# Optimization experiments

Measured on AMD Instinct MI355X. Metric: run time of the kernel, lower is better.

## Reference

```python
import jax, jax.numpy as jnp
import numpy as np

N_NODES = 100000
N_EDGES = 1600000
N_GRAPHS = 1000
HID = 64
NEG_SLOPE = 0.2


def _glorot(key, shape):
    fan_in, fan_out = shape[0], shape[-1]
    lim = float(np.sqrt(6.0 / (fan_in + fan_out)))
    return jax.random.uniform(key, shape, jnp.float32, -lim, lim)


def setup_inputs() -> dict:
    key = jax.random.key(0)
    ks = jax.random.split(key, 20)
    x = jax.random.normal(ks[0], (N_NODES, 1), jnp.float32)
    edge_index = jax.random.randint(ks[1], (2, N_EDGES), 0, N_NODES, jnp.int64)
    batch = jnp.sort(jax.random.randint(ks[2], (N_NODES,), 0, N_GRAPHS, jnp.int64))
    inp = {"x": x, "edge_index": edge_index, "batch": batch}
    # GATv2Conv layer 1 (in=3 -> out=HID, 1 head)
    inp["Wl1"] = _glorot(ks[3], (3, HID)); inp["bl1"] = jnp.zeros((HID,), jnp.float32)
    inp["Wr1"] = _glorot(ks[4], (3, HID)); inp["br1"] = jnp.zeros((HID,), jnp.float32)
    inp["a1"] = _glorot(ks[5], (HID, 1))[:, 0]; inp["b1"] = jnp.zeros((HID,), jnp.float32)
    # GATv2Conv layer 2 (HID -> HID)
    inp["Wl2"] = _glorot(ks[6], (HID, HID)); inp["bl2"] = jnp.zeros((HID,), jnp.float32)
    inp["Wr2"] = _glorot(ks[7], (HID, HID)); inp["br2"] = jnp.zeros((HID,), jnp.float32)
    inp["a2"] = _glorot(ks[8], (HID, 1))[:, 0]; inp["b2"] = jnp.zeros((HID,), jnp.float32)
    # lin2 (HID -> 2)
    inp["W3"] = _glorot(ks[9], (HID, 2)); inp["b3"] = jnp.zeros((2,), jnp.float32)
    return inp


def gatv2_layer(x, src, dst, Wl, bl, Wr, br, a, b):
    """GATv2Conv, 1 head, add_self_loops=True, negative_slope=0.2."""
    n = x.shape[0]
    xl = x @ Wl + bl  # source-side transform [N, C]
    xr = x @ Wr + br  # target-side transform [N, C]
    loops = jnp.arange(n, dtype=src.dtype)
    s = jnp.concatenate([src, loops])
    d = jnp.concatenate([dst, loops])
    # per-edge attention logit: a^T LeakyReLU(xl[j] + xr[i])
    e = jax.nn.leaky_relu(xl[s] + xr[d], NEG_SLOPE) @ a  # [E+N]
    # segment softmax over incoming edges of each dst node
    m = jax.ops.segment_max(e, d, num_segments=n)
    ex = jnp.exp(e - m[d])
    denom = jax.ops.segment_sum(ex, d, num_segments=n)
    alpha = ex / denom[d]
    out = jax.ops.segment_sum(alpha[:, None] * xl[s], d, num_segments=n)
    return out + b


def reference(x, edge_index, batch, Wl1, bl1, Wr1, br1, a1, b1,
              Wl2, bl2, Wr2, br2, a2, b2, W3, b3):
    n = x.shape[0]
    src, dst = edge_index[0], edge_index[1]
    ones = jnp.ones((src.shape[0],), jnp.float32)
    deg_in = jax.ops.segment_sum(ones, dst, num_segments=n)   # bincount(dst)
    deg_out = jax.ops.segment_sum(ones, src, num_segments=n)  # bincount(src)
    h = jnp.concatenate([x, deg_in[:, None], deg_out[:, None]], axis=1)  # [N,3]
    h = gatv2_layer(h, src, dst, Wl1, bl1, Wr1, br1, a1, b1)
    h = jnp.tanh(h)
    h = gatv2_layer(h, src, dst, Wl2, bl2, Wr2, br2, a2, b2)
    # global_max_pool over graphs
    g = jax.ops.segment_max(h, batch, num_segments=N_GRAPHS)  # [G, HID]
    return g @ W3 + b3  # [G, 2]
```

## Files before the change

### kernel.cpp

```cpp
#include <hip/hip_runtime.h>
#include <hip/hip_bf16.h>
#include <hip/hip_fp16.h>

#define HID 64
#define NEG_SLOPE 0.2f
#define BLK_E 4096
#define EDGE_CAP 6144
#define NDB 16

typedef _Float16 f16x2 __attribute__((ext_vector_type(2)));


__global__ void k_hist2(const int* __restrict__ src, const int* __restrict__ dst,
                        int* __restrict__ histS, int* __restrict__ histD,
                        int E, int NB, int NBLK) {
    __shared__ int hs[512], hd[512];
    int t = threadIdx.x, blk = blockIdx.x;
    for (int b = t; b < NB; b += 1024) { hs[b] = 0; hd[b] = 0; }
    __syncthreads();
    int base = blk * BLK_E;
    #pragma unroll
    for (int k = 0; k < BLK_E / 1024; ++k) {
        int i = base + k * 1024 + t;
        if (i < E) {
            atomicAdd(&hs[src[i] >> 8], 1);
            atomicAdd(&hd[dst[i] >> 8], 1);
        }
    }
    __syncthreads();
    for (int b = t; b < NB; b += 1024) {
        histS[b * NBLK + blk] = hs[b];
        histD[b * NBLK + blk] = hd[b];
    }
}

__global__ void k_binscan(int* __restrict__ histS, int* __restrict__ histD,
                          int* __restrict__ totS, int* __restrict__ totD,
                          int NB, int NBLK) {
    __shared__ int s[512];
    int b = blockIdx.x;
    int* hist = histS; int* tot = totS;
    if (b >= NB) { b -= NB; hist = histD; tot = totD; }
    int t = threadIdx.x;
    int v = (t < NBLK) ? hist[b * NBLK + t] : 0;
    s[t] = v;
    __syncthreads();
    for (int o = 1; o < 512; o <<= 1) {
        int u = (t >= o) ? s[t - o] : 0;
        __syncthreads();
        s[t] += u;
        __syncthreads();
    }
    if (t < NBLK) hist[b * NBLK + t] = s[t] - v;
    if (t == 511) tot[b] = s[511];
}

__global__ void k_binoffset(const int* __restrict__ totS, const int* __restrict__ totD,
                            int* __restrict__ bsS, int* __restrict__ bsD,
                            int NB, int E, int* __restrict__ row_off, int N) {
    __shared__ int s[512];
    int t = threadIdx.x;
    int v = (t < NB) ? totS[t] : 0;
    s[t] = v; __syncthreads();
    for (int o = 1; o < 512; o <<= 1) {
        int u = (t >= o) ? s[t - o] : 0;
        __syncthreads(); s[t] += u; __syncthreads();
    }
    if (t < NB) bsS[t] = s[t] - v;
    if (t == 0) bsS[NB] = E;
    __syncthreads();
    v = (t < NB) ? totD[t] : 0;
    s[t] = v; __syncthreads();
    for (int o = 1; o < 512; o <<= 1) {
        int u = (t >= o) ? s[t - o] : 0;
        __syncthreads(); s[t] += u; __syncthreads();
    }
    if (t < NB) bsD[t] = s[t] - v;
    if (t == 0) { bsD[NB] = E; row_off[N] = E; }
}

__global__ void k_scatter_bins(const int* __restrict__ src, const int* __restrict__ dst,
                               const int* __restrict__ histS, const int* __restrict__ histD,
                               const int* __restrict__ bsS, const int* __restrict__ bsD,
                               unsigned* __restrict__ packS, unsigned* __restrict__ packD,
                               int E, int NB, int NBLK) {
    __shared__ int baseS[512], baseD[512];
    int t = threadIdx.x, blk = blockIdx.x;
    for (int b = t; b < NB; b += 1024) {
        baseS[b] = bsS[b] + histS[b * NBLK + blk];
        baseD[b] = bsD[b] + histD[b * NBLK + blk];
    }
    __syncthreads();
    int base = blk * BLK_E;
    #pragma unroll
    for (int k = 0; k < BLK_E / 1024; ++k) {
        int i = base + k * 1024 + t;
        if (i < E) {
            int sv = src[i], dv = dst[i];
            int pD = atomicAdd(&baseD[dv >> 8], 1);
            packD[pD] = ((unsigned)(dv & 255) << 24) | (unsigned)sv;
            int pS = atomicAdd(&baseS[sv >> 8], 1);
            packS[pS] = (unsigned)(sv & 255);
        }
    }
}

__global__ void k_csr_bin_fused(const unsigned* __restrict__ packD, const int* __restrict__ bsD,
                                const unsigned* __restrict__ packS, const int* __restrict__ bsS,
                                int* __restrict__ row_off, float* __restrict__ deg_in,
                                int* __restrict__ csr_src,
                                const float* __restrict__ x,
                                const float* __restrict__ Wl, const float* __restrict__ bl,
                                const float* __restrict__ Wr, const float* __restrict__ br,
                                __half* __restrict__ A, __half* __restrict__ B, int N) {
    __shared__ int cnt[256], off[256], cur[256], cntS[256];
    __shared__ unsigned eb[EDGE_CAP];
    int b = blockIdx.x, t = threadIdx.x;
    int lo = bsD[b], hi = bsD[b + 1], ne = hi - lo;
    bool fits = (ne <= EDGE_CAP);
    if (t < 256) { cnt[t] = 0; cntS[t] = 0; }
    __syncthreads();
    for (int i = t; i < ne; i += 1024) {
        unsigned v = packD[lo + i];
        if (fits) eb[i] = v;
        atomicAdd(&cnt[v >> 24], 1);
    }
    int loS = bsS[b], hiS = bsS[b + 1];
    for (int i = loS + t; i < hiS; i += 1024) atomicAdd(&cntS[packS[i] & 255], 1);
    __syncthreads();
    if (t < 256) off[t] = cnt[t];
    __syncthreads();
    for (int o = 1; o < 256; o <<= 1) {
        int u = 0;
        if (t < 256 && t >= o) u = off[t - o];
        __syncthreads();
        if (t < 256) off[t] += u;
        __syncthreads();
    }
    if (t < 256) {
        int ex = off[t] - cnt[t];
        cur[t] = lo + ex;
        int node = b * 256 + t;
        if (node < N) {
            row_off[node] = lo + ex;
            deg_in[node] = (float)cnt[t];
        }
    }
    __syncthreads();
    for (int i = t; i < ne; i += 1024) {
        unsigned v = fits ? eb[i] : packD[lo + i];
        int pos = atomicAdd(&cur[v >> 24], 1);
        csr_src[pos] = (int)(v & 0xFFFFFFu);
    }
    int nd = b * 256 + (t >> 2);
    if (nd < N) {
        float h0 = x[nd];
        float h1 = (float)cnt[t >> 2];
        float h2 = (float)cntS[t >> 2];
        int c0 = (t & 3) * 16;
        unsigned ua[4], ub[4];
        #pragma unroll
        for (int p = 0; p < 2; ++p) {
            #pragma unroll
            for (int q = 0; q < 4; ++q) {
                int c = c0 + p * 8 + q * 2;
                float a0 = h0 * Wl[c]     + h1 * Wl[64 + c]     + h2 * Wl[128 + c]     + bl[c];
                float a1 = h0 * Wl[c + 1] + h1 * Wl[64 + c + 1] + h2 * Wl[128 + c + 1] + bl[c + 1];
                float b0 = h0 * Wr[c]     + h1 * Wr[64 + c]     + h2 * Wr[128 + c]     + br[c];
                float b1 = h0 * Wr[c + 1] + h1 * Wr[64 + c + 1] + h2 * Wr[128 + c + 1] + br[c + 1];
                f16x2 pa; pa.x = (_Float16)a0; pa.y = (_Float16)a1;
                f16x2 pb; pb.x = (_Float16)b0; pb.y = (_Float16)b1;
                ua[q] = __builtin_bit_cast(unsigned, pa);
                ub[q] = __builtin_bit_cast(unsigned, pb);
            }
            uint4 sa = make_uint4(ua[0], ua[1], ua[2], ua[3]);
            uint4 sb = make_uint4(ub[0], ub[1], ub[2], ub[3]);
            ((uint4*)A)[(size_t)nd * 8 + (t & 3) * 2 + p] = sa;
            ((uint4*)B)[(size_t)nd * 8 + (t & 3) * 2 + p] = sb;
        }
    }
}


__global__ void k_deghist(const float* __restrict__ deg_in, int* __restrict__ dhist, int N) {
    __shared__ int h[64];
    int t = threadIdx.x, b = blockIdx.x;
    if (t < 64) h[t] = 0;
    __syncthreads();
    int chunk = (N + NDB - 1) / NDB;
    int lo = b * chunk, hi = lo + chunk; if (hi > N) hi = N;
    for (int i = lo + t; i < hi; i += 1024) {
        int dg = (int)deg_in[i]; if (dg > 63) dg = 63;
        atomicAdd(&h[dg], 1);
    }
    __syncthreads();
    if (t < 64) dhist[t * NDB + b] = h[t];
}

__global__ void k_degscan(int* __restrict__ dhist) {
    __shared__ int s[1024];
    int t = threadIdx.x;
    int v = dhist[t];
    s[t] = v; __syncthreads();
    for (int o = 1; o < 1024; o <<= 1) {
        int u = (t >= o) ? s[t - o] : 0;
        __syncthreads(); s[t] += u; __syncthreads();
    }
    dhist[t] = s[t] - v;
}

__global__ void k_degscatter(const float* __restrict__ deg_in, const int* __restrict__ dhist,
                             int* __restrict__ perm, int N) {
    __shared__ int cur[64];
    int t = threadIdx.x, b = blockIdx.x;
    if (t < 64) cur[t] = dhist[t * NDB + b];
    __syncthreads();
    int chunk = (N + NDB - 1) / NDB;
    int lo = b * chunk, hi = lo + chunk; if (hi > N) hi = N;
    for (int i = lo + t; i < hi; i += 1024) {
        int dg = (int)deg_in[i]; if (dg > 63) dg = 63;
        int p = atomicAdd(&cur[dg], 1);
        perm[p] = i;
    }
}


struct H4 { f16x2 h[4]; };

__device__ __forceinline__ f16x2 bch2(unsigned u) {
    return __builtin_bit_cast(f16x2, u);
}

__device__ __forceinline__ H4 ld4(const uint4* __restrict__ T, size_t idx) {
    uint4 r = T[idx];
    H4 o;
    o.h[0] = bch2(r.x); o.h[1] = bch2(r.y); o.h[2] = bch2(r.z); o.h[3] = bch2(r.w);
    return o;
}

__device__ __forceinline__ float logit8(const H4& a, const H4& x,
                                        const float* __restrict__ awf, f16x2 ns2) {
    float t = 0.0f;
    #pragma unroll
    for (int j = 0; j < 4; ++j) {
        f16x2 s = a.h[j] + x.h[j];
        f16x2 l = __builtin_elementwise_max(s, ns2 * s);
        t = fmaf((float)l.x, awf[2 * j], t);
        t = fmaf((float)l.y, awf[2 * j + 1], t);
    }
    return t;
}

__device__ __forceinline__ void accum8(float* __restrict__ acc, const H4& a, float w) {
    #pragma unroll
    for (int j = 0; j < 4; ++j) {
        acc[2 * j]     = fmaf((float)a.h[j].x, w, acc[2 * j]);
        acc[2 * j + 1] = fmaf((float)a.h[j].y, w, acc[2 * j + 1]);
    }
}

template <typename OUT, bool TANH>
__global__ void k_gat_fused(const int* __restrict__ csr_src, const int* __restrict__ row_off,
                            const int* __restrict__ perm,
                            const __half* __restrict__ Ah, const __half* __restrict__ Bh,
                            const float* __restrict__ aw, const float* __restrict__ bias,
                            OUT* __restrict__ out, int N) {
    int tid = blockIdx.x * blockDim.x + threadIdx.x;
    int r = tid >> 3;
    int gl = threadIdx.x & 7;
    if (r >= N) return;
    int d = perm[N - 1 - r];

    const uint4* A16 = (const uint4*)Ah;
    const uint4* B16 = (const uint4*)Bh;
    f16x2 ns2;
    ns2.x = (_Float16)NEG_SLOPE; ns2.y = (_Float16)NEG_SLOPE;

    float awf[8], bw[8];
    {
        const float4* a4 = (const float4*)aw;
        const float4* b4 = (const float4*)bias;
        #pragma unroll
        for (int j = 0; j < 2; ++j) {
            float4 v = a4[gl * 2 + j];
            awf[4 * j] = v.x; awf[4 * j + 1] = v.y; awf[4 * j + 2] = v.z; awf[4 * j + 3] = v.w;
            float4 u = b4[gl * 2 + j];
            bw[4 * j] = u.x; bw[4 * j + 1] = u.y; bw[4 * j + 2] = u.z; bw[4 * j + 3] = u.w;
        }
    }

    size_t rowbase = (size_t)d * 8 + gl;
    H4 xh = ld4(B16, rowbase);
    H4 as = ld4(A16, rowbase);

    float t = logit8(as, xh, awf, ns2);
    t += __shfl_xor(t, 1); t += __shfl_xor(t, 2); t += __shfl_xor(t, 4);
    float m = t, denom = 1.0f;
    float acc[8];
    #pragma unroll
    for (int j = 0; j < 4; ++j) {
        acc[2 * j] = (float)as.h[j].x;
        acc[2 * j + 1] = (float)as.h[j].y;
    }

    int lo = row_off[d], hi = row_off[d + 1];
    int k = lo;
    for (; k + 3 < hi; k += 4) {
        int s0 = csr_src[k], s1 = csr_src[k + 1], s2 = csr_src[k + 2], s3 = csr_src[k + 3];
        H4 a0 = ld4(A16, (size_t)s0 * 8 + gl);
        H4 a1 = ld4(A16, (size_t)s1 * 8 + gl);
        H4 a2 = ld4(A16, (size_t)s2 * 8 + gl);
        H4 a3 = ld4(A16, (size_t)s3 * 8 + gl);
        float t0 = logit8(a0, xh, awf, ns2);
        float t1 = logit8(a1, xh, awf, ns2);
        float t2 = logit8(a2, xh, awf, ns2);
        float t3 = logit8(a3, xh, awf, ns2);
        t0 += __shfl_xor(t0, 1); t1 += __shfl_xor(t1, 1);
        t2 += __shfl_xor(t2, 1); t3 += __shfl_xor(t3, 1);
        t0 += __shfl_xor(t0, 2); t1 += __shfl_xor(t1, 2);
        t2 += __shfl_xor(t2, 2); t3 += __shfl_xor(t3, 2);
        t0 += __shfl_xor(t0, 4); t1 += __shfl_xor(t1, 4);
        t2 += __shfl_xor(t2, 4); t3 += __shfl_xor(t3, 4);
        float mx = fmaxf(fmaxf(t0, t1), fmaxf(t2, t3));
        if (mx > m) {
            float sc = __expf(m - mx);
            denom *= sc;
            #pragma unroll
            for (int j = 0; j < 8; ++j) acc[j] *= sc;
            m = mx;
        }
        float w0 = __expf(t0 - m), w1 = __expf(t1 - m);
        float w2 = __expf(t2 - m), w3 = __expf(t3 - m);
        denom += (w0 + w1) + (w2 + w3);
        accum8(acc, a0, w0);
        accum8(acc, a1, w1);
        accum8(acc, a2, w2);
        accum8(acc, a3, w3);
    }
    for (; k < hi; ++k) {
        int s0 = csr_src[k];
        H4 a0 = ld4(A16, (size_t)s0 * 8 + gl);
        float t0 = logit8(a0, xh, awf, ns2);
        t0 += __shfl_xor(t0, 1); t0 += __shfl_xor(t0, 2); t0 += __shfl_xor(t0, 4);
        if (t0 > m) {
            float sc = __expf(m - t0);
            denom *= sc;
            #pragma unroll
            for (int j = 0; j < 8; ++j) acc[j] *= sc;
            m = t0;
        }
        float w0 = __expf(t0 - m);
        denom += w0;
        accum8(acc, a0, w0);
    }

    float inv = 1.0f / denom;
    float v[8];
    #pragma unroll
    for (int j = 0; j < 8; ++j) {
        v[j] = acc[j] * inv + bw[j];
        if (TANH) v[j] = tanhf(v[j]);
    }
    if constexpr (sizeof(OUT) == 2) {
        unsigned u[4];
        #pragma unroll
        for (int j = 0; j < 4; ++j) {
            f16x2 p; p.x = (_Float16)v[2 * j]; p.y = (_Float16)v[2 * j + 1];
            u[j] = __builtin_bit_cast(unsigned, p);
        }
        ((uint4*)out)[(size_t)d * 8 + gl] = make_uint4(u[0], u[1], u[2], u[3]);
    } else {
        float4* o4 = (float4*)out;
        o4[(size_t)d * 16 + gl * 2]     = make_float4(v[0], v[1], v[2], v[3]);
        o4[(size_t)d * 16 + gl * 2 + 1] = make_float4(v[4], v[5], v[6], v[7]);
    }
}

__global__ __launch_bounds__(128) void k_xfrm2(
        const __half* __restrict__ H,
        const float* __restrict__ Wl, const float* __restrict__ bl,
        const float* __restrict__ Wr, const float* __restrict__ br,
        __half* __restrict__ A, __half* __restrict__ B, int N) {
    __shared__ float wls[4096];
    __shared__ float wrs[4096];
    __shared__ float bls[64], brs[64];
    int t = threadIdx.x;

    #pragma unroll
    for (int u = 0; u < 8; ++u) {
        ((float4*)wls)[t + 128 * u] = ((const float4*)Wl)[t + 128 * u];
        ((float4*)wrs)[t + 128 * u] = ((const float4*)Wr)[t + 128 * u];
    }
    if (t < 64) { bls[t] = bl[t]; brs[t] = br[t]; }
    __syncthreads();

    int node = blockIdx.x * 128 + t;
    if (node >= N) return;

    float hf[64];
    {
        const uint4* Hp = (const uint4*)(H + (size_t)node * HID);
        #pragma unroll
        for (int q = 0; q < 8; ++q) {
            uint4 rv = Hp[q];
            f16x2 p0 = bch2(rv.x), p1 = bch2(rv.y), p2 = bch2(rv.z), p3 = bch2(rv.w);
            hf[q * 8 + 0] = (float)p0.x; hf[q * 8 + 1] = (float)p0.y;
            hf[q * 8 + 2] = (float)p1.x; hf[q * 8 + 3] = (float)p1.y;
            hf[q * 8 + 4] = (float)p2.x; hf[q * 8 + 5] = (float)p2.y;
            hf[q * 8 + 6] = (float)p3.x; hf[q * 8 + 7] = (float)p3.y;
        }
    }

    #pragma unroll 1
    for (int cb = 0; cb < 8; ++cb) {
        const float* W  = (cb < 4) ? wls : wrs;
        const float* bb = (cb < 4) ? bls : brs;
        __half* OT      = (cb < 4) ? A : B;
        int c0 = (cb & 3) * 16;
        float acc[16] = {0, 0, 0, 0, 0, 0, 0, 0, 0, 0, 0, 0, 0, 0, 0, 0};
        #pragma unroll
        for (int kk = 0; kk < 64; ++kk) {
            float hv = hf[kk];
            const float4* wp = (const float4*)&W[kk * 64 + c0];
            float4 w0 = wp[0], w1 = wp[1], w2 = wp[2], w3 = wp[3];
            acc[0]  = fmaf(hv, w0.x, acc[0]);  acc[1]  = fmaf(hv, w0.y, acc[1]);
            acc[2]  = fmaf(hv, w0.z, acc[2]);  acc[3]  = fmaf(hv, w0.w, acc[3]);
            acc[4]  = fmaf(hv, w1.x, acc[4]);  acc[5]  = fmaf(hv, w1.y, acc[5]);
            acc[6]  = fmaf(hv, w1.z, acc[6]);  acc[7]  = fmaf(hv, w1.w, acc[7]);
            acc[8]  = fmaf(hv, w2.x, acc[8]);  acc[9]  = fmaf(hv, w2.y, acc[9]);
            acc[10] = fmaf(hv, w2.z, acc[10]); acc[11] = fmaf(hv, w2.w, acc[11]);
            acc[12] = fmaf(hv, w3.x, acc[12]); acc[13] = fmaf(hv, w3.y, acc[13]);
            acc[14] = fmaf(hv, w3.z, acc[14]); acc[15] = fmaf(hv, w3.w, acc[15]);
        }
        unsigned u[8];
        #pragma unroll
        for (int j = 0; j < 8; ++j) {
            f16x2 p;
            p.x = (_Float16)(acc[2 * j]     + bb[c0 + 2 * j]);
            p.y = (_Float16)(acc[2 * j + 1] + bb[c0 + 2 * j + 1]);
            u[j] = __builtin_bit_cast(unsigned, p);
        }
        uint4* op = (uint4*)(OT + (size_t)node * HID + c0);
        op[0] = make_uint4(u[0], u[1], u[2], u[3]);
        op[1] = make_uint4(u[4], u[5], u[6], u[7]);
    }
}

__global__ void k_pool_final(const float* __restrict__ C, const float* __restrict__ b2,
                             const int* __restrict__ batch,
                             const float* __restrict__ W3, const float* __restrict__ b3,
                             float* __restrict__ out, int N, int G) {
    int w = (int)((blockIdx.x * (size_t)blockDim.x + threadIdx.x) >> 6);
    int lane = threadIdx.x & 63;
    if (w >= G) return;
    int lo = 0, hi = N;
    while (lo < hi) { int mid = (lo + hi) >> 1; if (batch[mid] < w) lo = mid + 1; else hi = mid; }
    int s0 = lo;
    hi = N;
    while (lo < hi) { int mid = (lo + hi) >> 1; if (batch[mid] < w + 1) lo = mid + 1; else hi = mid; }
    int e0 = lo;

    float acc = -INFINITY;
    int i = s0;
    for (; i + 3 < e0; i += 4) {
        float v0 = C[(size_t)i * HID + lane];
        float v1 = C[(size_t)(i + 1) * HID + lane];
        float v2 = C[(size_t)(i + 2) * HID + lane];
        float v3 = C[(size_t)(i + 3) * HID + lane];
        acc = fmaxf(acc, fmaxf(fmaxf(v0, v1), fmaxf(v2, v3)));
    }
    for (; i < e0; ++i) acc = fmaxf(acc, C[(size_t)i * HID + lane]);
    float v = acc + b2[lane];

    float p0 = v * W3[lane * 2];
    float p1 = v * W3[lane * 2 + 1];
    #pragma unroll
    for (int o = 32; o; o >>= 1) { p0 += __shfl_xor(p0, o); p1 += __shfl_xor(p1, o); }
    if (lane == 0) {
        out[(size_t)w * 2]     = p0 + b3[0];
        out[(size_t)w * 2 + 1] = p1 + b3[1];
    }
}

extern "C" void kernel_launch(void* const* d_in, const int* in_sizes, int n_in,
                              void* d_out, int out_size, void* d_ws, size_t ws_size,
                              hipStream_t stream) {
    const float* x     = (const float*)d_in[0];
    const int*   ei    = (const int*)d_in[1];
    const int*   batch = (const int*)d_in[2];
    const float* Wl1 = (const float*)d_in[3];
    const float* bl1 = (const float*)d_in[4];
    const float* Wr1 = (const float*)d_in[5];
    const float* br1 = (const float*)d_in[6];
    const float* a1  = (const float*)d_in[7];
    const float* b1  = (const float*)d_in[8];
    const float* Wl2 = (const float*)d_in[9];
    const float* bl2 = (const float*)d_in[10];
    const float* Wr2 = (const float*)d_in[11];
    const float* br2 = (const float*)d_in[12];
    const float* a2  = (const float*)d_in[13];
    const float* b2  = (const float*)d_in[14];
    const float* W3  = (const float*)d_in[15];
    const float* b3  = (const float*)d_in[16];

    const int N = in_sizes[0];
    const int E = in_sizes[1] / 2;
    const int G = out_size / 2;
    const int NB = (N + 255) >> 8;
    const int NBLK = (E + BLK_E - 1) / BLK_E;

    float* ws = (float*)d_ws;
    size_t off = 0;
    float*  C  = ws + off; off += (size_t)N * HID;
    __half* Ah = (__half*)(ws + off); off += (size_t)N * HID / 2;
    __half* Bh = (__half*)(ws + off); off += (size_t)N * HID / 2;
    int*   row_off = (int*)(ws + off); off += N + 1;
    int*   csr_src = (int*)(ws + off); off += E;
    float* deg_in  = ws + off; off += N;
    int*   perm    = (int*)(ws + off); off += N;
    int*   dhist   = (int*)(ws + off); off += 1024;
    int*   bsS  = (int*)(ws + off); off += NB + 1;
    int*   bsD  = (int*)(ws + off); off += NB + 1;
    int*   totS = (int*)(ws + off); off += NB;
    int*   totD = (int*)(ws + off); off += NB;

    unsigned* packD = (unsigned*)C;
    unsigned* packS = packD + E;
    int* histS = (int*)(packS + E);
    int* histD = histS + (size_t)NB * NBLK;
    __half* Chalf = (__half*)C;

    const int* src  = ei;
    const int* dstp = ei + E;

    const int BT = 256;
    dim3 blk(BT);
    int grid_g8 = (int)(((size_t)N * 8 + BT - 1) / BT);
    int grid_x2 = (N + 127) / 128;

    k_hist2<<<NBLK, 1024, 0, stream>>>(src, dstp, histS, histD, E, NB, NBLK);
    k_binscan<<<2 * NB, 512, 0, stream>>>(histS, histD, totS, totD, NB, NBLK);
    k_binoffset<<<1, 512, 0, stream>>>(totS, totD, bsS, bsD, NB, E, row_off, N);
    k_scatter_bins<<<NBLK, 1024, 0, stream>>>(src, dstp, histS, histD, bsS, bsD,
                                              packS, packD, E, NB, NBLK);
    k_csr_bin_fused<<<NB, 1024, 0, stream>>>(packD, bsD, packS, bsS, row_off, deg_in,
                                             csr_src, x, Wl1, bl1, Wr1, br1, Ah, Bh, N);

    k_deghist<<<NDB, 1024, 0, stream>>>(deg_in, dhist, N);
    k_degscan<<<1, 1024, 0, stream>>>(dhist);
    k_degscatter<<<NDB, 1024, 0, stream>>>(deg_in, dhist, perm, N);

    k_gat_fused<__half, true><<<grid_g8, blk, 0, stream>>>(csr_src, row_off, perm,
                                                           Ah, Bh, a1, b1, Chalf, N);

    k_xfrm2<<<grid_x2, 128, 0, stream>>>(Chalf, Wl2, bl2, Wr2, br2, Ah, Bh, N);
    k_gat_fused<float, false><<<grid_g8, blk, 0, stream>>>(csr_src, row_off, perm,
                                                           Ah, Bh, a2, b2, C, N);

    k_pool_final<<<(G * 64 + BT - 1) / BT, blk, 0, stream>>>(C, b2, batch, W3, b3,
                                                             (float*)d_out, N, G);
}
```

Measured before the change: 225.0 us.

## Compute layer-2 node transforms with MFMA f16 matrix instructions

Replaces the scalar FMA-based 64x64 transform for layer 2 with a wave-level MFMA 16x16x32 f16 kernel, each wave handling 16 nodes. A small prep kernel transposes and converts Wl2/Wr2 to half precision so the B operands can be loaded as contiguous vectors. This aims to cut the ALU-bound per-node matmul cost. In exchange, weights are rounded to fp16, and outputs are written as scattered 2-byte stores instead of 16-byte vector stores.

```diff
diff --git a/kernel.cpp b/kernel.cpp
--- a/kernel.cpp
+++ b/kernel.cpp
@@ -9,6 +9,8 @@
 #define NDB 16
 
 typedef _Float16 f16x2 __attribute__((ext_vector_type(2)));
+typedef _Float16 f16x8 __attribute__((ext_vector_type(8)));
+typedef float f32x4 __attribute__((ext_vector_type(4)));
 
 
 __global__ void k_hist2(const int* __restrict__ src, const int* __restrict__ dst,
@@ -376,73 +378,54 @@
     }
 }
 
-__global__ __launch_bounds__(128) void k_xfrm2(
+
+__global__ void k_wprep(const float* __restrict__ Wl, const float* __restrict__ Wr,
+                        __half* __restrict__ Wtl, __half* __restrict__ Wtr) {
+    int t = blockIdx.x * blockDim.x + threadIdx.x;
+    if (t < 4096) {
+        int c = t & 63, k = t >> 6;
+        Wtl[(size_t)c * 64 + k] = __float2half(Wl[k * 64 + c]);
+        Wtr[(size_t)c * 64 + k] = __float2half(Wr[k * 64 + c]);
+    }
+}
+
+__global__ __launch_bounds__(256) void k_xfrm2_mfma(
         const __half* __restrict__ H,
-        const float* __restrict__ Wl, const float* __restrict__ bl,
-        const float* __restrict__ Wr, const float* __restrict__ br,
+        const __half* __restrict__ Wtl, const __half* __restrict__ Wtr,
+        const float* __restrict__ bl, const float* __restrict__ br,
         __half* __restrict__ A, __half* __restrict__ B, int N) {
-    __shared__ float wls[4096];
-    __shared__ float wrs[4096];
-    __shared__ float bls[64], brs[64];
-    int t = threadIdx.x;
-
-    #pragma unroll
-    for (int u = 0; u < 8; ++u) {
-        ((float4*)wls)[t + 128 * u] = ((const float4*)Wl)[t + 128 * u];
-        ((float4*)wrs)[t + 128 * u] = ((const float4*)Wr)[t + 128 * u];
-    }
-    if (t < 64) { bls[t] = bl[t]; brs[t] = br[t]; }
-    __syncthreads();
-
-    int node = blockIdx.x * 128 + t;
-    if (node >= N) return;
-
-    float hf[64];
-    {
-        const uint4* Hp = (const uint4*)(H + (size_t)node * HID);
+    int wid = threadIdx.x >> 6;
+    int lane = threadIdx.x & 63;
+    int n0 = (blockIdx.x * 4 + wid) * 16;
+    if (n0 >= N) return;
+    int row = lane & 15, kg = lane >> 4;
+    int nrow = n0 + row; if (nrow >= N) nrow = N - 1;
+
+    const uint4* Hp = (const uint4*)(H + (size_t)nrow * HID + kg * 8);
+    f16x8 af0 = __builtin_bit_cast(f16x8, Hp[0]);
+    f16x8 af1 = __builtin_bit_cast(f16x8, Hp[4]);
+
+    #pragma unroll
+    for (int tb = 0; tb < 2; ++tb) {
+        const __half* Wt = tb ? Wtr : Wtl;
+        const float* bb  = tb ? br : bl;
+        __half* OT       = tb ? B : A;
         #pragma unroll
-        for (int q = 0; q < 8; ++q) {
-            uint4 rv = Hp[q];
-            f16x2 p0 = bch2(rv.x), p1 = bch2(rv.y), p2 = bch2(rv.z), p3 = bch2(rv.w);
-            hf[q * 8 + 0] = (float)p0.x; hf[q * 8 + 1] = (float)p0.y;
-            hf[q * 8 + 2] = (float)p1.x; hf[q * 8 + 3] = (float)p1.y;
-            hf[q * 8 + 4] = (float)p2.x; hf[q * 8 + 5] = (float)p2.y;
-            hf[q * 8 + 6] = (float)p3.x; hf[q * 8 + 7] = (float)p3.y;
-        }
-    }
-
-    #pragma unroll 1
-    for (int cb = 0; cb < 8; ++cb) {
-        const float* W  = (cb < 4) ? wls : wrs;
-        const float* bb = (cb < 4) ? bls : brs;
-        __half* OT      = (cb < 4) ? A : B;
-        int c0 = (cb & 3) * 16;
-        float acc[16] = {0, 0, 0, 0, 0, 0, 0, 0, 0, 0, 0, 0, 0, 0, 0, 0};
-        #pragma unroll
-        for (int kk = 0; kk < 64; ++kk) {
-            float hv = hf[kk];
-            const float4* wp = (const float4*)&W[kk * 64 + c0];
-            float4 w0 = wp[0], w1 = wp[1], w2 = wp[2], w3 = wp[3];
-            acc[0]  = fmaf(hv, w0.x, acc[0]);  acc[1]  = fmaf(hv, w0.y, acc[1]);
-            acc[2]  = fmaf(hv, w0.z, acc[2]);  acc[3]  = fmaf(hv, w0.w, acc[3]);
-            acc[4]  = fmaf(hv, w1.x, acc[4]);  acc[5]  = fmaf(hv, w1.y, acc[5]);
-            acc[6]  = fmaf(hv, w1.z, acc[6]);  acc[7]  = fmaf(hv, w1.w, acc[7]);
-            acc[8]  = fmaf(hv, w2.x, acc[8]);  acc[9]  = fmaf(hv, w2.y, acc[9]);
-            acc[10] = fmaf(hv, w2.z, acc[10]); acc[11] = fmaf(hv, w2.w, acc[11]);
-            acc[12] = fmaf(hv, w3.x, acc[12]); acc[13] = fmaf(hv, w3.y, acc[13]);
-            acc[14] = fmaf(hv, w3.z, acc[14]); acc[15] = fmaf(hv, w3.w, acc[15]);
-        }
-        unsigned u[8];
-        #pragma unroll
-        for (int j = 0; j < 8; ++j) {
-            f16x2 p;
-            p.x = (_Float16)(acc[2 * j]     + bb[c0 + 2 * j]);
-            p.y = (_Float16)(acc[2 * j + 1] + bb[c0 + 2 * j + 1]);
-            u[j] = __builtin_bit_cast(unsigned, p);
-        }
-        uint4* op = (uint4*)(OT + (size_t)node * HID + c0);
-        op[0] = make_uint4(u[0], u[1], u[2], u[3]);
-        op[1] = make_uint4(u[4], u[5], u[6], u[7]);
+        for (int ct = 0; ct < 4; ++ct) {
+            int c = ct * 16 + row;
+            const uint4* Wp = (const uint4*)(Wt + (size_t)c * HID + kg * 8);
+            f16x8 bf0 = __builtin_bit_cast(f16x8, Wp[0]);
+            f16x8 bf1 = __builtin_bit_cast(f16x8, Wp[4]);
+            f32x4 acc = {0.f, 0.f, 0.f, 0.f};
+            acc = __builtin_amdgcn_mfma_f32_16x16x32_f16(af0, bf0, acc, 0, 0, 0);
+            acc = __builtin_amdgcn_mfma_f32_16x16x32_f16(af1, bf1, acc, 0, 0, 0);
+            float bias = bb[c];
+            #pragma unroll
+            for (int r = 0; r < 4; ++r) {
+                int node = n0 + kg * 4 + r;
+                if (node < N) OT[(size_t)node * HID + c] = __float2half(acc[r] + bias);
+            }
+        }
     }
 }
 
@@ -523,6 +506,9 @@
     int*   bsD  = (int*)(ws + off); off += NB + 1;
     int*   totS = (int*)(ws + off); off += NB;
     int*   totD = (int*)(ws + off); off += NB;
+    off = (off + 3) & ~(size_t)3;
+    __half* Wtl = (__half*)(ws + off); off += 2048;
+    __half* Wtr = (__half*)(ws + off); off += 2048;
 
     unsigned* packD = (unsigned*)C;
     unsigned* packS = packD + E;
@@ -536,7 +522,7 @@
     const int BT = 256;
     dim3 blk(BT);
     int grid_g8 = (int)(((size_t)N * 8 + BT - 1) / BT);
-    int grid_x2 = (N + 127) / 128;
+    int grid_mf = (N + 63) / 64;
 
     k_hist2<<<NBLK, 1024, 0, stream>>>(src, dstp, histS, histD, E, NB, NBLK);
     k_binscan<<<2 * NB, 512, 0, stream>>>(histS, histD, totS, totD, NB, NBLK);
@@ -549,11 +535,12 @@
     k_deghist<<<NDB, 1024, 0, stream>>>(deg_in, dhist, N);
     k_degscan<<<1, 1024, 0, stream>>>(dhist);
     k_degscatter<<<NDB, 1024, 0, stream>>>(deg_in, dhist, perm, N);
+    k_wprep<<<16, 256, 0, stream>>>(Wl2, Wr2, Wtl, Wtr);
 
     k_gat_fused<__half, true><<<grid_g8, blk, 0, stream>>>(csr_src, row_off, perm,
                                                            Ah, Bh, a1, b1, Chalf, N);
 
-    k_xfrm2<<<grid_x2, 128, 0, stream>>>(Chalf, Wl2, bl2, Wr2, br2, Ah, Bh, N);
+    k_xfrm2_mfma<<<grid_mf, 256, 0, stream>>>(Chalf, Wtl, Wtr, bl2, br2, Ah, Bh, N);
     k_gat_fused<float, false><<<grid_g8, blk, 0, stream>>>(csr_src, row_off, perm,
                                                            Ah, Bh, a2, b2, C, N);
 
```

Measured after the change: 203.7 us. 9.5% less time.
